# Kernel tuning notes

Measured on AMD Instinct MI355X. Metric: run time of the kernel, lower is better.

The kernel has to match this reference:

```python
import jax, jax.numpy as jnp
import numpy as np

BATCH, SEQ, CH, ORDER = 4, 8192, 512, 64


def setup_inputs() -> dict:
    key = jax.random.key(0)
    k1, k2, k3 = jax.random.split(key, 3)
    x = jax.random.normal(k1, (BATCH, SEQ, CH), dtype=jnp.float32)
    # RTF parameters: small init so the denominator polynomial 1 + sum a_i z^-i
    # stays well-conditioned (stable transfer function), as in the FSSM init.
    A = 0.01 * jax.random.normal(k2, (CH, ORDER), dtype=jnp.float32)
    B = 0.01 * jax.random.normal(k3, (CH, ORDER), dtype=jnp.float32)
    h0 = jnp.zeros((1,), dtype=jnp.float32)
    return {"x": x, "A": A, "B": B, "h0": h0}


def _rtf_kernel(A, B, L):
    # Evaluate H(z) = b(z)/a(z) at the L roots of unity, then irfft -> impulse response.
    C = A.shape[0]
    a = jnp.concatenate([jnp.ones((C, 1), A.dtype), A], axis=-1)  # (C, N+1), leading coeff 1
    a_f = jnp.fft.rfft(a, n=L, axis=-1)                           # (C, L//2+1)
    b_f = jnp.fft.rfft(B, n=L, axis=-1)
    return jnp.fft.irfft(b_f / a_f, n=L, axis=-1)                 # (C, L)


def reference(x, A, B, h0):
    Bt, L, C = x.shape
    K = _rtf_kernel(A, B, L)                                      # (C, L)
    n_fft = 2 * L                                                 # causal (linear) convolution
    x_f = jnp.fft.rfft(x, n=n_fft, axis=1)                        # (B, n_fft//2+1, C)
    k_f = jnp.fft.rfft(K, n=n_fft, axis=-1).T[None]               # (1, n_fft//2+1, C)
    h1 = jnp.fft.irfft(x_f * k_f, n=n_fft, axis=1)[:, :L]         # (B, L, C)
    y1 = h1 + h0 * x
    return jax.nn.gelu(y1)
```

## Files before the change

kernel.cpp:

```cpp
#include <hip/hip_runtime.h>
#include <stdint.h>

#define NBATCH 4
#define LSEQ   8192
#define CH     512
#define ORDER  64
#define KTAP   256

typedef _Float16 half8 __attribute__((ext_vector_type(8)));
typedef _Float16 half4 __attribute__((ext_vector_type(4)));
typedef float    f32x4 __attribute__((ext_vector_type(4)));

#define PADP  8512
#define PAD0  279
#define NW    9

#define AFRAG_HALFS  ((size_t)CH * NW * 64 * 8)
#define XT_HALFS     ((size_t)CH * NBATCH * PADP)
#define WS_NEED      ((AFRAG_HALFS + XT_HALFS) * 2)

#define NAPREP 128
#define NXPOSE (133 * 8 * NBATCH)

#define XROWB 2624
#define SMEMB (16 * XROWB)
#define LOWB  1040

__global__ __launch_bounds__(256) void prep(const float* __restrict__ A,
                                            const float* __restrict__ B,
                                            const float* __restrict__ h0,
                                            const float* __restrict__ x,
                                            _Float16* __restrict__ afr,
                                            _Float16* __restrict__ xT) {
    __shared__ float    Ksh[4][KTAP];
    __shared__ _Float16 tile[64][74];
    const int bid = blockIdx.x;
    if (bid < NAPREP) {
        const int wv = threadIdx.x >> 6, lane = threadIdx.x & 63;
        const int c  = bid * 4 + wv;
        const float a  = A[c * ORDER + lane];
        const float bc = B[c * ORDER + lane];
        const float h0v = h0[0];
        float s = 0.0f;
        for (int t = 0; t < KTAP; ++t) {
            const float s1 = __shfl(s, 0);
            const float bt = (t < ORDER) ? __shfl(bc, t) : 0.0f;
            const float y  = bt + s1;
            float su = __shfl_down(s, 1);
            if (lane == ORDER - 1) su = 0.0f;
            s = su - a * y;
            if (lane == 0) Ksh[wv][t] = (t == 0) ? (y + h0v) : y;
        }
        __syncthreads();
        const int i = lane & 15, g = lane >> 4;
        for (int w = 0; w < NW; ++w) {
            half8 hv;
#pragma unroll
            for (int e = 0; e < 8; ++e) {
                const int t = 32 * w + 15 + i - 8 * g - e;
                hv[e] = (_Float16)((t >= 0 && t < KTAP) ? Ksh[wv][t] : 0.0f);
            }
            *reinterpret_cast<half8*>(afr + ((size_t)(c * NW + w) * 64 + lane) * 8) = hv;
        }
    } else {
        const int bid2 = bid - NAPREP;
        const int px   = bid2 % 133;
        const int cy   = (bid2 / 133) & 7;
        const int bz   = bid2 / (133 * 8);
        const int p0 = px * 64, c0 = cy * 64, t = threadIdx.x;
        const int cl = (t & 15) * 4;
        const int rl = t >> 4;
#pragma unroll
        for (int pass = 0; pass < 4; ++pass) {
            const int pl = rl + 16 * pass;
            const int r  = p0 + pl - PAD0;
            float4 v = {0.0f, 0.0f, 0.0f, 0.0f};
            if (r >= 0 && r < LSEQ)
                v = *reinterpret_cast<const float4*>(x + ((size_t)bz * LSEQ + r) * CH + c0 + cl);
            tile[pl][cl + 0] = (_Float16)v.x;
            tile[pl][cl + 1] = (_Float16)v.y;
            tile[pl][cl + 2] = (_Float16)v.z;
            tile[pl][cl + 3] = (_Float16)v.w;
        }
        __syncthreads();
        const int pl2 = (t & 15) * 4;
#pragma unroll
        for (int pass = 0; pass < 4; ++pass) {
            const int cc = (t >> 4) + 16 * pass;
            half4 hv;
#pragma unroll
            for (int d = 0; d < 4; ++d) hv[d] = tile[pl2 + d][cc];
            *reinterpret_cast<half4*>(xT + ((size_t)((c0 + cc) * NBATCH + bz)) * PADP + p0 + pl2) = hv;
        }
    }
}

__global__ __launch_bounds__(256) void fir_mfma(const _Float16* __restrict__ xT,
                                                const _Float16* __restrict__ afr,
                                                float* __restrict__ out) {
    __shared__ __align__(16) char smem[SMEMB];
    const int gid     = blockIdx.x;
    const int logical = (gid & 7) * 128 + (gid >> 3);
    const int chgrp   = logical >> 5;
    const int rem     = logical & 31;
    const int bb      = rem >> 3;
    const int tg      = rem & 7;

    {
        const int grp = threadIdx.x >> 4;
        const int l16 = threadIdx.x & 15;
        const size_t rowbase = ((size_t)(chgrp * 16 + grp) * NBATCH + bb) * PADP
                             + (size_t)tg * 1024 + 8;
#pragma unroll
        for (int it = 0; it < 11; ++it) {
            const int chunk = l16 + 16 * it;
            if (chunk < 164) {
                const half8 v = *reinterpret_cast<const half8*>(xT + rowbase + (size_t)chunk * 8);
                *reinterpret_cast<half8*>(smem + (size_t)grp * XROWB + chunk * 16) = v;
            }
        }
    }
    __syncthreads();

    const int wid = threadIdx.x >> 6, lane = threadIdx.x & 63;
    const int j = lane & 15, g = lane >> 4;
    const int c0 = chgrp * 16 + wid * 4;
    const _Float16* af = afr + (size_t)lane * 8;

    f32x4 acc[4][4];
#pragma unroll
    for (int ti = 0; ti < 4; ++ti)
#pragma unroll
        for (int q = 0; q < 4; ++q) acc[ti][q] = (f32x4){0.f, 0.f, 0.f, 0.f};

#pragma unroll
    for (int w = 0; w < NW; ++w) {
        half8 a[4];
#pragma unroll
        for (int q = 0; q < 4; ++q)
            a[q] = *reinterpret_cast<const half8*>(af + (size_t)((c0 + q) * NW + w) * 512);
        const int base = 16 * j + 8 * g - 32 * w + 256;
#pragma unroll
        for (int ti = 0; ti < 4; ++ti) {
#pragma unroll
            for (int q = 0; q < 4; ++q) {
                const half8 bv = *reinterpret_cast<const half8*>(
                    smem + (size_t)(wid * 4 + q) * XROWB + 2 * (base + 256 * ti));
                acc[ti][q] = __builtin_amdgcn_mfma_f32_16x16x32_f16(a[q], bv, acc[ti][q], 0, 0, 0);
            }
        }
    }

    const int cq  = threadIdx.x & 3;
    const int nr0 = threadIdx.x >> 2;
#pragma unroll
    for (int ti = 0; ti < 4; ++ti) {
        __syncthreads();
#pragma unroll
        for (int q = 0; q < 4; ++q) {
            f32x4 o;
#pragma unroll
            for (int r = 0; r < 4; ++r) {
                const float y  = acc[ti][q][r];
                const float wv = fmaf(y * y, 0.14270963f, 1.5957691f);
                const float e  = __expf(y * wv);
                o[r] = y - y * __builtin_amdgcn_rcpf(e + 1.0f);
            }
            *reinterpret_cast<f32x4*>(smem + (size_t)(wid * 4 + q) * LOWB
                                      + 4 * (16 * j + 4 * g)) = o;
        }
        __syncthreads();
        float* obp = out + ((size_t)bb * LSEQ + tg * 1024 + ti * 256) * CH + chgrp * 16 + 4 * cq;
#pragma unroll
        for (int it = 0; it < 4; ++it) {
            const int n = nr0 + 64 * it;
            f32x4 o;
            o[0] = *reinterpret_cast<const float*>(smem + (size_t)(4 * cq + 0) * LOWB + 4 * n);
            o[1] = *reinterpret_cast<const float*>(smem + (size_t)(4 * cq + 1) * LOWB + 4 * n);
            o[2] = *reinterpret_cast<const float*>(smem + (size_t)(4 * cq + 2) * LOWB + 4 * n);
            o[3] = *reinterpret_cast<const float*>(smem + (size_t)(4 * cq + 3) * LOWB + 4 * n);
            *reinterpret_cast<f32x4*>(obp + (size_t)n * CH) = o;
        }
    }
}

#define RINGF 32
#define CPBF  256
__global__ __launch_bounds__(ORDER) void rtf_impulse_fb(const float* __restrict__ A,
                                                        const float* __restrict__ B,
                                                        const float* __restrict__ h0,
                                                        float* __restrict__ kt4) {
    const int c = blockIdx.x, lane = threadIdx.x;
    const float a = A[c * ORDER + lane], bc = B[c * ORDER + lane], h0v = h0[0];
    float s = 0.0f;
    for (int t = 0; t < KTAP; ++t) {
        const float s1 = __shfl(s, 0);
        const float bt = (t < ORDER) ? __shfl(bc, t) : 0.0f;
        const float y  = bt + s1;
        float su = __shfl_down(s, 1);
        if (lane == ORDER - 1) su = 0.0f;
        s = su - a * y;
        if (lane == 0) kt4[((size_t)(t >> 2) * CH + c) * 4 + (t & 3)] = (t == 0) ? (y + h0v) : y;
    }
}
__global__ __launch_bounds__(CPBF) void fir_gelu_fb(const float* __restrict__ x,
                                                    const float* __restrict__ kt4,
                                                    float* __restrict__ out) {
    const int h = blockIdx.x;
    const int logical = ((h & 7) << 8) | (h >> 3);
    const int tile = logical & 255, sl = logical >> 8;
    const int cb = sl & 1, b = sl >> 1;
    const int c = cb * CPBF + threadIdx.x;
    const int n0 = tile * RINGF;
    const float* xb = x + (size_t)b * LSEQ * CH + c;
    const float4* kt4v = (const float4*)kt4;
    float acc[RINGF]; float ring[RINGF]; float px[2][8]; float kbuf[2][8];
#pragma unroll
    for (int r = 0; r < RINGF; ++r) acc[r] = 0.0f;
#pragma unroll
    for (int i = 0; i < RINGF; ++i) ring[i] = xb[(size_t)(n0 + i) * CH];
    {
        const float4 ka = kt4v[(size_t)0 * CH + c];
        const float4 kb = kt4v[(size_t)1 * CH + c];
        kbuf[0][0] = ka.x; kbuf[0][1] = ka.y; kbuf[0][2] = ka.z; kbuf[0][3] = ka.w;
        kbuf[0][4] = kb.x; kbuf[0][5] = kb.y; kbuf[0][6] = kb.z; kbuf[0][7] = kb.w;
#pragma unroll
        for (int g2 = 0; g2 < 8; ++g2) {
            const int m = n0 - 1 - g2;
            px[0][g2] = (m >= 0) ? xb[(size_t)m * CH] : 0.0f;
        }
    }
    for (int tb = 0; tb < KTAP; tb += RINGF) {
#pragma unroll
        for (int qq = 0; qq < 4; ++qq) {
            const int cur = qq & 1, nxt = cur ^ 1;
            const int tn = tb + 8 * (qq + 1);
            if (tn < KTAP) {
                const float4 ka = kt4v[(size_t)(tn >> 2) * CH + c];
                const float4 kb = kt4v[(size_t)((tn >> 2) + 1) * CH + c];
                kbuf[nxt][0] = ka.x; kbuf[nxt][1] = ka.y; kbuf[nxt][2] = ka.z; kbuf[nxt][3] = ka.w;
                kbuf[nxt][4] = kb.x; kbuf[nxt][5] = kb.y; kbuf[nxt][6] = kb.z; kbuf[nxt][7] = kb.w;
#pragma unroll
                for (int g2 = 0; g2 < 8; ++g2) {
                    const int m = n0 - tn - 1 - g2;
                    px[nxt][g2] = (m >= 0) ? xb[(size_t)m * CH] : 0.0f;
                }
            }
#pragma unroll
            for (int g2 = 0; g2 < 8; ++g2) {
                const int tq = 8 * qq + g2;
                const float kv = kbuf[cur][g2];
#pragma unroll
                for (int r = 0; r < RINGF; ++r)
                    acc[r] = fmaf(kv, ring[(r - tq) & (RINGF - 1)], acc[r]);
                ring[(RINGF - 1 - tq) & (RINGF - 1)] = px[cur][g2];
            }
        }
    }
    float* ob = out + ((size_t)b * LSEQ + n0) * CH + c;
#pragma unroll
    for (int r = 0; r < RINGF; ++r) {
        const float y = acc[r];
        const float wv = fmaf(y * y, 0.14270963f, 1.5957691f);
        const float e = __expf(y * wv);
        ob[(size_t)r * CH] = y - y * __builtin_amdgcn_rcpf(e + 1.0f);
    }
}

extern "C" void kernel_launch(void* const* d_in, const int* in_sizes, int n_in,
                              void* d_out, int out_size, void* d_ws, size_t ws_size,
                              hipStream_t stream) {
    const float* x  = (const float*)d_in[0];
    const float* A  = (const float*)d_in[1];
    const float* B  = (const float*)d_in[2];
    const float* h0 = (const float*)d_in[3];
    float* out = (float*)d_out;

    if (ws_size >= WS_NEED) {
        _Float16* afr = (_Float16*)d_ws;
        _Float16* xT  = afr + AFRAG_HALFS;
        prep<<<dim3(NAPREP + NXPOSE), dim3(256), 0, stream>>>(A, B, h0, x, afr, xT);
        fir_mfma<<<dim3(1024), dim3(256), 0, stream>>>(xT, afr, out);
    } else {
        float* kt4 = (float*)d_ws;
        rtf_impulse_fb<<<dim3(CH), dim3(ORDER), 0, stream>>>(A, B, h0, kt4);
        fir_gelu_fb<<<dim3((LSEQ / RINGF) * (CH / CPBF) * NBATCH), dim3(CPBF), 0, stream>>>(x, kt4, out);
    }
}
```

Before: 60.16 us.

## Switch Toeplitz convolution MFMA to 32x32x16 tiles with swizzled LDS layout

```diff
diff --git a/kernel.cpp b/kernel.cpp
--- a/kernel.cpp
+++ b/kernel.cpp
@@ -7,24 +7,27 @@
 #define ORDER  64
 #define KTAP   256
 
-typedef _Float16 half8 __attribute__((ext_vector_type(8)));
-typedef _Float16 half4 __attribute__((ext_vector_type(4)));
-typedef float    f32x4 __attribute__((ext_vector_type(4)));
+typedef _Float16 half8  __attribute__((ext_vector_type(8)));
+typedef _Float16 half4  __attribute__((ext_vector_type(4)));
+typedef float    f32x4  __attribute__((ext_vector_type(4)));
+typedef float    f32x16 __attribute__((ext_vector_type(16)));
 
 #define PADP  8512
 #define PAD0  279
-#define NW    9
-
-#define AFRAG_HALFS  ((size_t)CH * NW * 64 * 8)
+#define NW2   18
+
+#define AFRAG_HALFS  ((size_t)CH * NW2 * 64 * 8)
 #define XT_HALFS     ((size_t)CH * NBATCH * PADP)
 #define WS_NEED      ((AFRAG_HALFS + XT_HALFS) * 2)
 
 #define NAPREP 128
 #define NXPOSE (133 * 8 * NBATCH)
 
-#define XROWB 2624
+#define XROWB 2752
 #define SMEMB (16 * XROWB)
 #define LOWB  1040
+
+__device__ __forceinline__ int swz(int b) { return b ^ (((b >> 7) & 7) << 4); }
 
 __global__ __launch_bounds__(256) void prep(const float* __restrict__ A,
                                             const float* __restrict__ B,
@@ -52,15 +55,15 @@
             if (lane == 0) Ksh[wv][t] = (t == 0) ? (y + h0v) : y;
         }
         __syncthreads();
-        const int i = lane & 15, g = lane >> 4;
-        for (int w = 0; w < NW; ++w) {
+        const int i32 = lane & 31, h = lane >> 5;
+        for (int w = 0; w < NW2; ++w) {
             half8 hv;
 #pragma unroll
             for (int e = 0; e < 8; ++e) {
-                const int t = 32 * w + 15 + i - 8 * g - e;
+                const int t = 16 * w - 17 + i32 - 8 * h - e;
                 hv[e] = (_Float16)((t >= 0 && t < KTAP) ? Ksh[wv][t] : 0.0f);
             }
-            *reinterpret_cast<half8*>(afr + ((size_t)(c * NW + w) * 64 + lane) * 8) = hv;
+            *reinterpret_cast<half8*>(afr + ((size_t)(c * NW2 + w) * 64 + lane) * 8) = hv;
         }
     } else {
         const int bid2 = bid - NAPREP;
@@ -116,38 +119,32 @@
             const int chunk = l16 + 16 * it;
             if (chunk < 164) {
                 const half8 v = *reinterpret_cast<const half8*>(xT + rowbase + (size_t)chunk * 8);
-                *reinterpret_cast<half8*>(smem + (size_t)grp * XROWB + chunk * 16) = v;
+                *reinterpret_cast<half8*>(smem + (size_t)grp * XROWB + swz(chunk * 16)) = v;
             }
         }
     }
     __syncthreads();
 
     const int wid = threadIdx.x >> 6, lane = threadIdx.x & 63;
-    const int j = lane & 15, g = lane >> 4;
+    const int j32 = lane & 31, h = lane >> 5;
     const int c0 = chgrp * 16 + wid * 4;
-    const _Float16* af = afr + (size_t)lane * 8;
-
-    f32x4 acc[4][4];
-#pragma unroll
-    for (int ti = 0; ti < 4; ++ti)
-#pragma unroll
-        for (int q = 0; q < 4; ++q) acc[ti][q] = (f32x4){0.f, 0.f, 0.f, 0.f};
-
-#pragma unroll
-    for (int w = 0; w < NW; ++w) {
-        half8 a[4];
-#pragma unroll
-        for (int q = 0; q < 4; ++q)
-            a[q] = *reinterpret_cast<const half8*>(af + (size_t)((c0 + q) * NW + w) * 512);
-        const int base = 16 * j + 8 * g - 32 * w + 256;
-#pragma unroll
-        for (int ti = 0; ti < 4; ++ti) {
-#pragma unroll
-            for (int q = 0; q < 4; ++q) {
-                const half8 bv = *reinterpret_cast<const half8*>(
-                    smem + (size_t)(wid * 4 + q) * XROWB + 2 * (base + 256 * ti));
-                acc[ti][q] = __builtin_amdgcn_mfma_f32_16x16x32_f16(a[q], bv, acc[ti][q], 0, 0, 0);
-            }
+
+    f32x16 acc[4];
+#pragma unroll
+    for (int q = 0; q < 4; ++q)
+#pragma unroll
+        for (int r = 0; r < 16; ++r) acc[q][r] = 0.0f;
+
+#pragma unroll
+    for (int w = 0; w < NW2; ++w) {
+        const int bir = swz(576 - 32 * w + 64 * j32 + 16 * h);
+#pragma unroll
+        for (int q = 0; q < 4; ++q) {
+            const half8 a = *reinterpret_cast<const half8*>(
+                afr + ((size_t)((c0 + q) * NW2 + w) * 64 + lane) * 8);
+            const half8 bv = *reinterpret_cast<const half8*>(
+                smem + (size_t)(wid * 4 + q) * XROWB + bir);
+            acc[q] = __builtin_amdgcn_mfma_f32_32x32x16_f16(a, bv, acc[q], 0, 0, 0);
         }
     }
 
@@ -156,18 +153,23 @@
 #pragma unroll
     for (int ti = 0; ti < 4; ++ti) {
         __syncthreads();
-#pragma unroll
-        for (int q = 0; q < 4; ++q) {
-            f32x4 o;
-#pragma unroll
-            for (int r = 0; r < 4; ++r) {
-                const float y  = acc[ti][q][r];
-                const float wv = fmaf(y * y, 0.14270963f, 1.5957691f);
-                const float e  = __expf(y * wv);
-                o[r] = y - y * __builtin_amdgcn_rcpf(e + 1.0f);
-            }
-            *reinterpret_cast<f32x4*>(smem + (size_t)(wid * 4 + q) * LOWB
-                                      + 4 * (16 * j + 4 * g)) = o;
+        if ((j32 >> 3) == ti) {
+#pragma unroll
+            for (int q = 0; q < 4; ++q) {
+#pragma unroll
+                for (int rg = 0; rg < 4; ++rg) {
+                    f32x4 o;
+#pragma unroll
+                    for (int r = 0; r < 4; ++r) {
+                        const float y  = acc[q][4 * rg + r];
+                        const float wv = fmaf(y * y, 0.14270963f, 1.5957691f);
+                        const float e  = __expf(y * wv);
+                        o[r] = y - y * __builtin_amdgcn_rcpf(e + 1.0f);
+                    }
+                    *reinterpret_cast<f32x4*>(smem + (size_t)(wid * 4 + q) * LOWB
+                                              + 4 * (32 * (j32 & 7) + 8 * rg + 4 * h)) = o;
+                }
+            }
         }
         __syncthreads();
         float* obp = out + ((size_t)bb * LSEQ + tg * 1024 + ti * 256) * CH + chgrp * 16 + 4 * cq;
```

Result: slower. 73.67 us (+22.4%).
